# Performance work log

Hardware: AMD Instinct MI355X
Metric: run time of the kernel (lower is better)

## Reference

```python
import jax, jax.numpy as jnp
import numpy as np

N_NODES = 100000
N_EDGES = 3200000
N_FEAT = 128
N_GRAPHS = 256
N_CLASSES = 10


def setup_inputs() -> dict:
    key = jax.random.key(0)
    ks = jax.random.split(key, 10)
    x = jax.random.normal(ks[0], (N_NODES, N_FEAT), dtype=jnp.float32)
    edge_index = jax.random.randint(ks[1], (2, N_EDGES), 0, N_NODES, dtype=jnp.int64)
    batch = jnp.sort(jax.random.randint(ks[2], (N_NODES,), 0, N_GRAPHS, dtype=jnp.int64))
    # GCNConv weights (glorot-ish scaling) and biases
    W1 = jax.random.normal(ks[3], (N_FEAT, 16), dtype=jnp.float32) / np.sqrt(N_FEAT)
    b1 = jnp.zeros((16,), dtype=jnp.float32)
    W2 = jax.random.normal(ks[4], (16, 32), dtype=jnp.float32) / np.sqrt(16.0)
    b2 = jnp.zeros((32,), dtype=jnp.float32)
    Wfc = jax.random.normal(ks[5], (32, N_CLASSES), dtype=jnp.float32) / np.sqrt(32.0)
    bfc = jnp.zeros((N_CLASSES,), dtype=jnp.float32)
    return {"x": x, "edge_index": edge_index, "batch": batch,
            "W1": W1, "b1": b1, "W2": W2, "b2": b2, "Wfc": Wfc, "bfc": bfc}


def reference(x, edge_index, batch, W1, b1, W2, b2, Wfc, bfc):
    N = x.shape[0]
    # --- GCN normalization with self-loops (PyG GCNConv default) ---
    loop = jnp.arange(N, dtype=edge_index.dtype)
    src = jnp.concatenate([edge_index[0], loop])  # [E+N]
    dst = jnp.concatenate([edge_index[1], loop])  # [E+N]
    ones = jnp.ones_like(src, dtype=x.dtype)
    deg = jax.ops.segment_sum(ones, dst, num_segments=N)  # in-degree incl self-loop
    dinv = jax.lax.rsqrt(deg)  # deg >= 1 thanks to self-loops
    norm = dinv[src] * dinv[dst]  # [E+N]

    def gcn_conv(h, W, b):
        h = h @ W                               # [N, out] linear first (small out dim)
        msg = h[src] * norm[:, None]            # gather + edge-wise scale
        agg = jax.ops.segment_sum(msg, dst, num_segments=N)  # scatter-add
        return agg + b

    h = jax.nn.relu(gcn_conv(x, W1, b1))
    h = jax.nn.relu(gcn_conv(h, W2, b2))

    # --- global mean pool over graphs ---
    g_sum = jax.ops.segment_sum(h, batch, num_segments=N_GRAPHS)  # [G, 32]
    g_cnt = jax.ops.segment_sum(jnp.ones((N,), dtype=h.dtype), batch, num_segments=N_GRAPHS)
    pooled = g_sum / jnp.maximum(g_cnt, 1.0)[:, None]

    return pooled @ Wfc + bfc  # [G, num_classes]
```

## Files before the change

### kernel.cpp

```cpp
#include <hip/hip_runtime.h>
#include <hip/hip_fp16.h>

#define NF   128
#define C1   16
#define C2   32
#define NCLS 10
#define BSH  8
#define BN   256
#define MAXB 512
#define S    9216
#define TILE 4096
#define CAP  12288


__global__ __launch_bounds__(512) void k_bin(const int* __restrict__ ei,
                                             int* __restrict__ packed,
                                             int* __restrict__ offmat,
                                             int E, int nbuck) {
    __shared__ int hist[MAXB];
    __shared__ int off0[MAXB];
    __shared__ int cur[MAXB];
    int tid = threadIdx.x;
    long long t0 = (long long)blockIdx.x * TILE;

    for (int i = tid; i < MAXB; i += 512) hist[i] = 0;
    __syncthreads();

    long long eb = t0 + (long long)tid * 8;
    int src[8], dst[8];
    if (eb + 8 <= E) {
        const int4* s4 = (const int4*)(ei + eb);
        const int4* d4 = (const int4*)(ei + E + eb);
        int4 a = s4[0], b = s4[1], c = d4[0], d = d4[1];
        src[0]=a.x; src[1]=a.y; src[2]=a.z; src[3]=a.w;
        src[4]=b.x; src[5]=b.y; src[6]=b.z; src[7]=b.w;
        dst[0]=c.x; dst[1]=c.y; dst[2]=c.z; dst[3]=c.w;
        dst[4]=d.x; dst[5]=d.y; dst[6]=d.z; dst[7]=d.w;
    } else {
#pragma unroll
        for (int u = 0; u < 8; ++u) {
            long long e = eb + u;
            src[u] = (e < E) ? ei[e] : 0;
            dst[u] = (e < E) ? ei[E + e] : -1;
        }
    }
#pragma unroll
    for (int u = 0; u < 8; ++u)
        if (dst[u] >= 0) atomicAdd(&hist[dst[u] >> BSH], 1);
    __syncthreads();
    if (tid < 64) {
        int carry = 0;
        for (int c = 0; c < MAXB / 64; ++c) {
            int idx = c * 64 + tid;
            int v = hist[idx];
            int orig = v;
            for (int off = 1; off < 64; off <<= 1) {
                int t = __shfl_up(v, off);
                if (tid >= off) v += t;
            }
            int ex = v - orig + carry;
            off0[idx] = ex;
            cur[idx] = ex;
            carry += __shfl(v, 63);
        }
    }
    __syncthreads();
    int* orow = offmat + (size_t)blockIdx.x * (nbuck + 1);
    for (int b = tid; b <= nbuck; b += 512) orow[b] = off0[b];
#pragma unroll
    for (int u = 0; u < 8; ++u) {
        int d = dst[u];
        if (d >= 0) {
            int b = d >> BSH;
            int slot = atomicAdd(&cur[b], 1);
            packed[t0 + slot] = src[u] | ((d & (BN - 1)) << 17);
        }
    }
}


__global__ __launch_bounds__(1024) void k_csr(const int* __restrict__ packed,
                                              const int* __restrict__ offmat,
                                              int* __restrict__ csr,
                                              int* __restrict__ rowptr,
                                              int* __restrict__ deg,
                                              float* __restrict__ dinv,
                                              int N, int nbuck, int nblkA) {
    __shared__ int stage[CAP];
    __shared__ int startA[1024];
    __shared__ int o1A[1024];
    __shared__ int hcnt[BN];
    __shared__ int cur[BN];
    __shared__ int wsum[16];
    __shared__ int woff[4];
    int tid = threadIdx.x;
    int wid = tid >> 6, lane = tid & 63;
    int b = blockIdx.x;
    size_t base = (size_t)b * S;

    int len = 0, o1 = 0;
    if (tid < nblkA) {
        const int* orow = offmat + (size_t)tid * (nbuck + 1) + b;
        o1 = orow[0];
        len = orow[1] - o1;
    }
    o1A[tid] = o1;
    if (tid < BN) hcnt[tid] = 0;

    int v = len;
#pragma unroll
    for (int off = 1; off < 64; off <<= 1) {
        int t = __shfl_up(v, off);
        if (lane >= off) v += t;
    }
    if (lane == 63) wsum[wid] = v;
    __syncthreads();
    if (tid < 16) {
        int w = wsum[tid];
#pragma unroll
        for (int off = 1; off < 16; off <<= 1) {
            int t = __shfl_up(w, off);
            if (tid >= off) w += t;
        }
        wsum[tid] = w;
    }
    __syncthreads();
    int m = wsum[15];
    int incl = v + ((wid > 0) ? wsum[wid - 1] : 0);
    startA[tid] = incl - len;
    __syncthreads();
    if (m > CAP) m = CAP;

    for (int i = tid; i < m; i += 1024) {
        int lo = 0, hi = 1023;
        while (lo < hi) {
            int mid = (lo + hi + 1) >> 1;
            if (startA[mid] <= i) lo = mid; else hi = mid - 1;
        }
        int p = packed[(size_t)lo * TILE + o1A[lo] + (i - startA[lo])];
        stage[i] = p;
        atomicAdd(&hcnt[p >> 17], 1);
    }
    __syncthreads();
    int v2 = (tid < BN) ? hcnt[tid] : 0;
    int s2 = v2;
#pragma unroll
    for (int off = 1; off < 64; off <<= 1) {
        int t = __shfl_up(s2, off);
        if (lane >= off) s2 += t;
    }
    if (tid < BN && lane == 63) wsum[wid] = s2;
    __syncthreads();
    if (tid == 0) {
        int acc = 0;
#pragma unroll
        for (int k = 0; k < 4; ++k) { int t = wsum[k]; woff[k] = acc; acc += t; }
    }
    __syncthreads();
    if (tid < BN) {
        int ex = (s2 - v2) + woff[wid];
        cur[tid] = ex;
        int n = (b << BSH) + tid;
        if (n < N) {
            rowptr[n] = (int)base + ex;
            deg[n] = v2;
            dinv[n] = rsqrtf((float)v2 + 1.0f);
        }
    }
    __syncthreads();
    for (int i = tid; i < m; i += 1024) {
        int p = stage[i];
        int slot = atomicAdd(&cur[p >> 17], 1);
        csr[base + slot] = p & 0x1FFFF;
    }
}


__global__ __launch_bounds__(256) void k_lin1(const float* __restrict__ x,
                                              const float* __restrict__ W1,
                                              const float* __restrict__ dinv,
                                              __half* __restrict__ y1h, int N) {
    __shared__ float ws[NF * C1];
    __shared__ float xs[16 * 132];
    int tid = threadIdx.x;
    for (int t = tid; t < NF * C1; t += 256) ws[t] = W1[t];
    int n0 = blockIdx.x * 16;
    const float4* x4 = (const float4*)x;
    for (int t = tid; t < 16 * 32; t += 256) {
        int r = t >> 5, c = t & 31;
        int n = n0 + r;
        float4 v = (n < N) ? x4[(size_t)n * 32 + c] : make_float4(0.f, 0.f, 0.f, 0.f);
        float* d = &xs[r * 132 + c * 4];
        d[0] = v.x; d[1] = v.y; d[2] = v.z; d[3] = v.w;
    }
    __syncthreads();
    int r = tid >> 4, j = tid & 15;
    float acc = 0.0f;
#pragma unroll 4
    for (int k = 0; k < NF; ++k) acc += xs[r * 132 + k] * ws[k * C1 + j];
    int n = n0 + r;
    if (n < N) y1h[(size_t)n * C1 + j] = __float2half_rn(acc * dinv[n]);
}


template <int MODE>
__global__ __launch_bounds__(256) void k_gather_h(const int* __restrict__ rowptr,
                                                  const int* __restrict__ deg,
                                                  const int* __restrict__ csr,
                                                  const float* __restrict__ dinv,
                                                  const float* __restrict__ bias,
                                                  const __half2* __restrict__ yh,
                                                  void* __restrict__ outp, int N) {
    int tid = threadIdx.x;
    int j = tid & 7;
    int n = blockIdx.x * 32 + (tid >> 3);
    if (n >= N) return;
    int k0 = rowptr[n];
    int k1 = k0 + deg[n];
    float2 self = __half22float2(yh[(size_t)n * 8 + j]);
    float a0 = self.x, a1 = self.y;
    float e0 = 0.f, e1 = 0.f, f0 = 0.f, f1 = 0.f, g0 = 0.f, g1 = 0.f;
    int k = k0;
    for (; k + 7 < k1; k += 8) {
        int my = csr[k + j];
        int s0 = __shfl(my, 0, 8), s1 = __shfl(my, 1, 8);
        int s2 = __shfl(my, 2, 8), s3 = __shfl(my, 3, 8);
        int s4 = __shfl(my, 4, 8), s5 = __shfl(my, 5, 8);
        int s6 = __shfl(my, 6, 8), s7 = __shfl(my, 7, 8);
        float2 v0 = __half22float2(yh[(size_t)s0 * 8 + j]);
        float2 v1 = __half22float2(yh[(size_t)s1 * 8 + j]);
        float2 v2 = __half22float2(yh[(size_t)s2 * 8 + j]);
        float2 v3 = __half22float2(yh[(size_t)s3 * 8 + j]);
        float2 v4 = __half22float2(yh[(size_t)s4 * 8 + j]);
        float2 v5 = __half22float2(yh[(size_t)s5 * 8 + j]);
        float2 v6 = __half22float2(yh[(size_t)s6 * 8 + j]);
        float2 v7 = __half22float2(yh[(size_t)s7 * 8 + j]);
        a0 += v0.x + v4.x; a1 += v0.y + v4.y;
        e0 += v1.x + v5.x; e1 += v1.y + v5.y;
        f0 += v2.x + v6.x; f1 += v2.y + v6.y;
        g0 += v3.x + v7.x; g1 += v3.y + v7.y;
    }
    for (; k < k1; ++k) {
        float2 v = __half22float2(yh[(size_t)csr[k] * 8 + j]);
        a0 += v.x; a1 += v.y;
    }
    float dn = dinv[n];
    float rx = dn * ((a0 + e0) + (f0 + g0));
    float ry = dn * ((a1 + e1) + (f1 + g1));
    if (MODE == 0) {
        ((float2*)outp)[(size_t)n * 8 + j] = make_float2(rx, ry);
    } else {
        float2 bb = ((const float2*)bias)[j];
        float u0 = fmaxf(rx + bb.x, 0.0f) * dn;
        float u1 = fmaxf(ry + bb.y, 0.0f) * dn;
        ((__half2*)outp)[(size_t)n * 8 + j] = __floats2half2_rn(u0, u1);
    }
}


__global__ __launch_bounds__(256) void k_pool_fc(const float* __restrict__ z,
                                                 const float* __restrict__ W2,
                                                 const float* __restrict__ b2,
                                                 const int* __restrict__ batch,
                                                 const float* __restrict__ Wfc,
                                                 const float* __restrict__ bfc,
                                                 float* __restrict__ out, int N, int G) {
    __shared__ float W2s[C1 * C2];
    int tid = threadIdx.x;
    for (int t = tid; t < C1 * C2; t += 256) W2s[t] = W2[t];

    int g = blockIdx.x;
    int lo = 0, hi = N;
    while (lo < hi) { int m = (lo + hi) >> 1; if (batch[m] < g) lo = m + 1; else hi = m; }
    int start = lo;
    lo = start; hi = N;
    while (lo < hi) { int m = (lo + hi) >> 1; if (batch[m] < g + 1) lo = m + 1; else hi = m; }
    int end = lo;
    __syncthreads();

    int i = tid & 31, r = tid >> 5;
    float bi = b2[i];
    float acc = 0.0f;
    for (int n = start + r; n < end; n += 8) {
        const float* zr = &z[(size_t)n * C1];
        float h = bi;
#pragma unroll
        for (int j = 0; j < C1; ++j) h += zr[j] * W2s[j * C2 + i];
        acc += fmaxf(h, 0.0f);
    }

    __shared__ float red[256];
    red[tid] = acc;
    __syncthreads();
    for (int s = 4; s >= 1; s >>= 1) {
        if (r < s) red[tid] += red[tid + s * 32];
        __syncthreads();
    }
    __shared__ float pooled[C2];
    if (tid < C2) {
        float cnt = (float)(end - start);
        pooled[tid] = red[tid] / fmaxf(cnt, 1.0f);
    }
    __syncthreads();
    if (tid < NCLS) {
        float a = bfc[tid];
#pragma unroll
        for (int j = 0; j < C2; ++j) a += pooled[j] * Wfc[j * NCLS + tid];
        out[g * NCLS + tid] = a;
    }
}

extern "C" void kernel_launch(void* const* d_in, const int* in_sizes, int n_in,
                              void* d_out, int out_size, void* d_ws, size_t ws_size,
                              hipStream_t stream) {
    const float* x    = (const float*)d_in[0];
    const int*   ei   = (const int*)d_in[1];
    const int*   batch= (const int*)d_in[2];
    const float* W1   = (const float*)d_in[3];
    const float* b1   = (const float*)d_in[4];
    const float* W2   = (const float*)d_in[5];
    const float* b2   = (const float*)d_in[6];
    const float* Wfc  = (const float*)d_in[7];
    const float* bfc  = (const float*)d_in[8];
    float* out = (float*)d_out;

    const int N = in_sizes[0] / NF;
    const int E = in_sizes[1] / 2;
    const int G = out_size / NCLS;
    const int nbuck = (N + BN - 1) >> BSH;
    const int nblkA = (E + TILE - 1) / TILE;

    char* p = (char*)d_ws;
    auto alloc = [&](size_t bytes) { char* q = p; p += (bytes + 63) & ~(size_t)63; return q; };
    int*     rowptr  = (int*)    alloc((size_t)N * 4);
    int*     deg     = (int*)    alloc((size_t)N * 4);
    float*   dinv    = (float*)  alloc((size_t)N * 4);
    int*     packed  = (int*)    alloc((size_t)nblkA * TILE * 4);
    int*     offmat  = (int*)    alloc((size_t)nblkA * (nbuck + 1) * 4);
    int*     csr     = (int*)    alloc((size_t)nbuck * S * 4);
    __half*  y1h     = (__half*) alloc((size_t)N * C1 * 2);
    __half*  uh      = (__half*) alloc((size_t)N * C1 * 2);
    float*   z       = (float*)  alloc((size_t)N * C1 * 4);

    k_bin<<<nblkA, 512, 0, stream>>>(ei, packed, offmat, E, nbuck);
    k_csr<<<nbuck, 1024, 0, stream>>>(packed, offmat, csr, rowptr, deg, dinv,
                                      N, nbuck, nblkA);

    k_lin1<<<(N + 15) / 16, 256, 0, stream>>>(x, W1, dinv, y1h, N);
    k_gather_h<1><<<(N + 31) / 32, 256, 0, stream>>>(rowptr, deg, csr, dinv, b1,
                                                     (const __half2*)y1h, uh, N);
    k_gather_h<0><<<(N + 31) / 32, 256, 0, stream>>>(rowptr, deg, csr, dinv, b1,
                                                     (const __half2*)uh, z, N);

    k_pool_fc<<<G, 256, 0, stream>>>(z, W2, b2, batch, Wfc, bfc, out, N, G);
}
```

Before: 160.4 us.

## Fuse second GCN gather with W2 linear and graph pooling via atomics

The second gather kernel now also applies W2, bias and ReLU in registers and shared memory, then accumulates per-graph sums with segmented atomic adds. This removes the fp32 z intermediate and its write and re-read by a separate pool kernel, which had serialized per-graph work across only G blocks. A small single-block kernel then divides by node counts and applies the final FC layer. The first gather also gets a 16-wide unrolled loop for more loads in flight. Atomic float adds make the summation order nondeterministic, and the extra memset and launch add small overhead.

Result: faster. 152.8 us (-4.7%).

```diff
diff --git a/kernel.cpp b/kernel.cpp
--- a/kernel.cpp
+++ b/kernel.cpp
@@ -203,14 +203,13 @@
 }
 
 
-template <int MODE>
-__global__ __launch_bounds__(256) void k_gather_h(const int* __restrict__ rowptr,
-                                                  const int* __restrict__ deg,
-                                                  const int* __restrict__ csr,
-                                                  const float* __restrict__ dinv,
-                                                  const float* __restrict__ bias,
-                                                  const __half2* __restrict__ yh,
-                                                  void* __restrict__ outp, int N) {
+__global__ __launch_bounds__(256) void k_gather1(const int* __restrict__ rowptr,
+                                                 const int* __restrict__ deg,
+                                                 const int* __restrict__ csr,
+                                                 const float* __restrict__ dinv,
+                                                 const float* __restrict__ bias,
+                                                 const __half2* __restrict__ yh,
+                                                 __half2* __restrict__ outp, int N) {
     int tid = threadIdx.x;
     int j = tid & 7;
     int n = blockIdx.x * 32 + (tid >> 3);
@@ -221,12 +220,38 @@
     float a0 = self.x, a1 = self.y;
     float e0 = 0.f, e1 = 0.f, f0 = 0.f, f1 = 0.f, g0 = 0.f, g1 = 0.f;
     int k = k0;
+    for (; k + 15 < k1; k += 16) {
+        int mA = csr[k + j];
+        int mB = csr[k + 8 + j];
+        int s0 = __shfl(mA, 0, 8), s1 = __shfl(mA, 1, 8), s2 = __shfl(mA, 2, 8), s3 = __shfl(mA, 3, 8);
+        int s4 = __shfl(mA, 4, 8), s5 = __shfl(mA, 5, 8), s6 = __shfl(mA, 6, 8), s7 = __shfl(mA, 7, 8);
+        int t0 = __shfl(mB, 0, 8), t1 = __shfl(mB, 1, 8), t2 = __shfl(mB, 2, 8), t3 = __shfl(mB, 3, 8);
+        int t4 = __shfl(mB, 4, 8), t5 = __shfl(mB, 5, 8), t6 = __shfl(mB, 6, 8), t7 = __shfl(mB, 7, 8);
+        float2 v0 = __half22float2(yh[(size_t)s0 * 8 + j]);
+        float2 v1 = __half22float2(yh[(size_t)s1 * 8 + j]);
+        float2 v2 = __half22float2(yh[(size_t)s2 * 8 + j]);
+        float2 v3 = __half22float2(yh[(size_t)s3 * 8 + j]);
+        float2 v4 = __half22float2(yh[(size_t)s4 * 8 + j]);
+        float2 v5 = __half22float2(yh[(size_t)s5 * 8 + j]);
+        float2 v6 = __half22float2(yh[(size_t)s6 * 8 + j]);
+        float2 v7 = __half22float2(yh[(size_t)s7 * 8 + j]);
+        float2 w0 = __half22float2(yh[(size_t)t0 * 8 + j]);
+        float2 w1 = __half22float2(yh[(size_t)t1 * 8 + j]);
+        float2 w2 = __half22float2(yh[(size_t)t2 * 8 + j]);
+        float2 w3 = __half22float2(yh[(size_t)t3 * 8 + j]);
+        float2 w4 = __half22float2(yh[(size_t)t4 * 8 + j]);
+        float2 w5 = __half22float2(yh[(size_t)t5 * 8 + j]);
+        float2 w6 = __half22float2(yh[(size_t)t6 * 8 + j]);
+        float2 w7 = __half22float2(yh[(size_t)t7 * 8 + j]);
+        a0 += (v0.x + v4.x) + (w0.x + w4.x); a1 += (v0.y + v4.y) + (w0.y + w4.y);
+        e0 += (v1.x + v5.x) + (w1.x + w5.x); e1 += (v1.y + v5.y) + (w1.y + w5.y);
+        f0 += (v2.x + v6.x) + (w2.x + w6.x); f1 += (v2.y + v6.y) + (w2.y + w6.y);
+        g0 += (v3.x + v7.x) + (w3.x + w7.x); g1 += (v3.y + v7.y) + (w3.y + w7.y);
+    }
     for (; k + 7 < k1; k += 8) {
         int my = csr[k + j];
-        int s0 = __shfl(my, 0, 8), s1 = __shfl(my, 1, 8);
-        int s2 = __shfl(my, 2, 8), s3 = __shfl(my, 3, 8);
-        int s4 = __shfl(my, 4, 8), s5 = __shfl(my, 5, 8);
-        int s6 = __shfl(my, 6, 8), s7 = __shfl(my, 7, 8);
+        int s0 = __shfl(my, 0, 8), s1 = __shfl(my, 1, 8), s2 = __shfl(my, 2, 8), s3 = __shfl(my, 3, 8);
+        int s4 = __shfl(my, 4, 8), s5 = __shfl(my, 5, 8), s6 = __shfl(my, 6, 8), s7 = __shfl(my, 7, 8);
         float2 v0 = __half22float2(yh[(size_t)s0 * 8 + j]);
         float2 v1 = __half22float2(yh[(size_t)s1 * 8 + j]);
         float2 v2 = __half22float2(yh[(size_t)s2 * 8 + j]);
@@ -247,66 +272,119 @@
     float dn = dinv[n];
     float rx = dn * ((a0 + e0) + (f0 + g0));
     float ry = dn * ((a1 + e1) + (f1 + g1));
-    if (MODE == 0) {
-        ((float2*)outp)[(size_t)n * 8 + j] = make_float2(rx, ry);
-    } else {
-        float2 bb = ((const float2*)bias)[j];
-        float u0 = fmaxf(rx + bb.x, 0.0f) * dn;
-        float u1 = fmaxf(ry + bb.y, 0.0f) * dn;
-        ((__half2*)outp)[(size_t)n * 8 + j] = __floats2half2_rn(u0, u1);
-    }
-}
-
-
-__global__ __launch_bounds__(256) void k_pool_fc(const float* __restrict__ z,
-                                                 const float* __restrict__ W2,
-                                                 const float* __restrict__ b2,
-                                                 const int* __restrict__ batch,
-                                                 const float* __restrict__ Wfc,
-                                                 const float* __restrict__ bfc,
-                                                 float* __restrict__ out, int N, int G) {
+    float2 bb = ((const float2*)bias)[j];
+    float u0 = fmaxf(rx + bb.x, 0.0f) * dn;
+    float u1 = fmaxf(ry + bb.y, 0.0f) * dn;
+    outp[(size_t)n * 8 + j] = __floats2half2_rn(u0, u1);
+}
+
+
+__global__ __launch_bounds__(256) void k_gather_pool(const int* __restrict__ rowptr,
+                                                     const int* __restrict__ deg,
+                                                     const int* __restrict__ csr,
+                                                     const float* __restrict__ dinv,
+                                                     const float* __restrict__ W2,
+                                                     const float* __restrict__ b2,
+                                                     const int* __restrict__ batch,
+                                                     const __half2* __restrict__ yh,
+                                                     float* __restrict__ g_sum, int N) {
     __shared__ float W2s[C1 * C2];
+    __shared__ float h2s[32][C2 + 1];
+    __shared__ int bb[32];
     int tid = threadIdx.x;
     for (int t = tid; t < C1 * C2; t += 256) W2s[t] = W2[t];
-
-    int g = blockIdx.x;
+    int n0 = blockIdx.x * 32;
+    if (tid < 32) bb[tid] = batch[min(n0 + tid, N - 1)];
+
+    int j = tid & 7;
+    int r = tid >> 3;
+    int n = n0 + r;
+    float rx = 0.f, ry = 0.f;
+    if (n < N) {
+        int k0 = rowptr[n];
+        int k1 = k0 + deg[n];
+        float2 self = __half22float2(yh[(size_t)n * 8 + j]);
+        float a0 = self.x, a1 = self.y;
+        float e0 = 0.f, e1 = 0.f, f0 = 0.f, f1 = 0.f, g0 = 0.f, g1 = 0.f;
+        int k = k0;
+        for (; k + 7 < k1; k += 8) {
+            int my = csr[k + j];
+            int s0 = __shfl(my, 0, 8), s1 = __shfl(my, 1, 8), s2 = __shfl(my, 2, 8), s3 = __shfl(my, 3, 8);
+            int s4 = __shfl(my, 4, 8), s5 = __shfl(my, 5, 8), s6 = __shfl(my, 6, 8), s7 = __shfl(my, 7, 8);
+            float2 v0 = __half22float2(yh[(size_t)s0 * 8 + j]);
+            float2 v1 = __half22float2(yh[(size_t)s1 * 8 + j]);
+            float2 v2 = __half22float2(yh[(size_t)s2 * 8 + j]);
+            float2 v3 = __half22float2(yh[(size_t)s3 * 8 + j]);
+            float2 v4 = __half22float2(yh[(size_t)s4 * 8 + j]);
+            float2 v5 = __half22float2(yh[(size_t)s5 * 8 + j]);
+            float2 v6 = __half22float2(yh[(size_t)s6 * 8 + j]);
+            float2 v7 = __half22float2(yh[(size_t)s7 * 8 + j]);
+            a0 += v0.x + v4.x; a1 += v0.y + v4.y;
+            e0 += v1.x + v5.x; e1 += v1.y + v5.y;
+            f0 += v2.x + v6.x; f1 += v2.y + v6.y;
+            g0 += v3.x + v7.x; g1 += v3.y + v7.y;
+        }
+        for (; k < k1; ++k) {
+            float2 v = __half22float2(yh[(size_t)csr[k] * 8 + j]);
+            a0 += v.x; a1 += v.y;
+        }
+        float dn = dinv[n];
+        rx = dn * ((a0 + e0) + (f0 + g0));
+        ry = dn * ((a1 + e1) + (f1 + g1));
+    }
+    __syncthreads();
+
+    float zf[16];
+#pragma unroll
+    for (int q = 0; q < 8; ++q) {
+        zf[2 * q]     = __shfl(rx, q, 8);
+        zf[2 * q + 1] = __shfl(ry, q, 8);
+    }
+#pragma unroll
+    for (int i = 0; i < 4; ++i) {
+        int c = 4 * j + i;
+        float p = 0.0f;
+#pragma unroll
+        for (int jj = 0; jj < C1; ++jj) p += zf[jj] * W2s[jj * C2 + c];
+        h2s[r][c] = (n < N) ? fmaxf(p + b2[c], 0.0f) : 0.0f;
+    }
+    __syncthreads();
+    if (tid < C2) {
+        int c = tid;
+        float s = 0.0f;
+        int cg = bb[0];
+        for (int rr = 0; rr < 32; ++rr) {
+            int g = bb[rr];
+            if (g != cg) { atomicAdd(&g_sum[(size_t)cg * C2 + c], s); s = 0.0f; cg = g; }
+            s += h2s[rr][c];
+        }
+        atomicAdd(&g_sum[(size_t)cg * C2 + c], s);
+    }
+}
+
+
+__global__ __launch_bounds__(256) void k_final(const float* __restrict__ g_sum,
+                                               const int* __restrict__ batch,
+                                               const float* __restrict__ Wfc,
+                                               const float* __restrict__ bfc,
+                                               float* __restrict__ out, int N, int G) {
+    int g = threadIdx.x;
+    if (g >= G) return;
     int lo = 0, hi = N;
     while (lo < hi) { int m = (lo + hi) >> 1; if (batch[m] < g) lo = m + 1; else hi = m; }
     int start = lo;
     lo = start; hi = N;
     while (lo < hi) { int m = (lo + hi) >> 1; if (batch[m] < g + 1) lo = m + 1; else hi = m; }
-    int end = lo;
-    __syncthreads();
-
-    int i = tid & 31, r = tid >> 5;
-    float bi = b2[i];
-    float acc = 0.0f;
-    for (int n = start + r; n < end; n += 8) {
-        const float* zr = &z[(size_t)n * C1];
-        float h = bi;
-#pragma unroll
-        for (int j = 0; j < C1; ++j) h += zr[j] * W2s[j * C2 + i];
-        acc += fmaxf(h, 0.0f);
-    }
-
-    __shared__ float red[256];
-    red[tid] = acc;
-    __syncthreads();
-    for (int s = 4; s >= 1; s >>= 1) {
-        if (r < s) red[tid] += red[tid + s * 32];
-        __syncthreads();
-    }
-    __shared__ float pooled[C2];
-    if (tid < C2) {
-        float cnt = (float)(end - start);
-        pooled[tid] = red[tid] / fmaxf(cnt, 1.0f);
-    }
-    __syncthreads();
-    if (tid < NCLS) {
-        float a = bfc[tid];
-#pragma unroll
-        for (int j = 0; j < C2; ++j) a += pooled[j] * Wfc[j * NCLS + tid];
-        out[g * NCLS + tid] = a;
+    float inv = 1.0f / fmaxf((float)(lo - start), 1.0f);
+    float pooled[C2];
+#pragma unroll
+    for (int jj = 0; jj < C2; ++jj) pooled[jj] = g_sum[(size_t)g * C2 + jj] * inv;
+#pragma unroll
+    for (int c = 0; c < NCLS; ++c) {
+        float a = bfc[c];
+#pragma unroll
+        for (int jj = 0; jj < C2; ++jj) a += pooled[jj] * Wfc[jj * NCLS + c];
+        out[g * NCLS + c] = a;
     }
 }
 
@@ -340,17 +418,17 @@
     int*     csr     = (int*)    alloc((size_t)nbuck * S * 4);
     __half*  y1h     = (__half*) alloc((size_t)N * C1 * 2);
     __half*  uh      = (__half*) alloc((size_t)N * C1 * 2);
-    float*   z       = (float*)  alloc((size_t)N * C1 * 4);
+    float*   g_sum   = (float*)  alloc((size_t)G * C2 * 4);
 
     k_bin<<<nblkA, 512, 0, stream>>>(ei, packed, offmat, E, nbuck);
+    hipMemsetAsync(g_sum, 0, (size_t)G * C2 * 4, stream);
     k_csr<<<nbuck, 1024, 0, stream>>>(packed, offmat, csr, rowptr, deg, dinv,
                                       N, nbuck, nblkA);
 
     k_lin1<<<(N + 15) / 16, 256, 0, stream>>>(x, W1, dinv, y1h, N);
-    k_gather_h<1><<<(N + 31) / 32, 256, 0, stream>>>(rowptr, deg, csr, dinv, b1,
-                                                     (const __half2*)y1h, uh, N);
-    k_gather_h<0><<<(N + 31) / 32, 256, 0, stream>>>(rowptr, deg, csr, dinv, b1,
-                                                     (const __half2*)uh, z, N);
-
-    k_pool_fc<<<G, 256, 0, stream>>>(z, W2, b2, batch, Wfc, bfc, out, N, G);
-}
+    k_gather1<<<(N + 31) / 32, 256, 0, stream>>>(rowptr, deg, csr, dinv, b1,
+                                                 (const __half2*)y1h, (__half2*)uh, N);
+    k_gather_pool<<<(N + 31) / 32, 256, 0, stream>>>(rowptr, deg, csr, dinv, W2, b2,
+                                                     batch, (const __half2*)uh, g_sum, N);
+    k_final<<<1, 256, 0, stream>>>(g_sum, batch, Wfc, bfc, out, N, G);
+}
```
